# Kernel tuning notes

Measured on AMD Instinct MI355X. Metric: run time of the kernel, lower is better.

Reference implementation:

```python
import jax, jax.numpy as jnp
import numpy as np

B, Q_LEN, HID = 4, 1024, 4096
N_HEADS, N_KV_HEADS, HEAD_DIM = 32, 8, 128
PAST_LEN = 1024
SCALING = 1.0  # wrapper's self.scaling (applied to query before SDPA)
NEG = jnp.float32(-1e9)


def setup_inputs() -> dict:
    key = jax.random.key(0)
    ks = jax.random.split(key, 10)
    return {
        "hidden_states": jax.random.normal(ks[0], (B, Q_LEN, HID), jnp.float32),
        "past_k": jax.random.normal(ks[1], (B, N_KV_HEADS, PAST_LEN, HEAD_DIM), jnp.float32),
        "past_v": jax.random.normal(ks[2], (B, N_KV_HEADS, PAST_LEN, HEAD_DIM), jnp.float32),
        # attention_mask semantics follow the wrapper's SDPA path: positions where
        # attention_mask == 0 are attended (mask_bool True), others masked out.
        "attention_mask": jnp.zeros((B, PAST_LEN + Q_LEN), jnp.int32),
        "Wq": jax.random.normal(ks[3], (HID, HID), jnp.float32) * 0.02,
        "bq": jnp.zeros((HID,), jnp.float32),
        "Wk": jax.random.normal(ks[4], (N_KV_HEADS * HEAD_DIM, HID), jnp.float32) * 0.02,
        "bk": jnp.zeros((N_KV_HEADS * HEAD_DIM,), jnp.float32),
        "Wv": jax.random.normal(ks[5], (N_KV_HEADS * HEAD_DIM, HID), jnp.float32) * 0.02,
        "bv": jnp.zeros((N_KV_HEADS * HEAD_DIM,), jnp.float32),
        "Wo": jax.random.normal(ks[6], (HID, HID), jnp.float32) * 0.02,
        "bo": jnp.zeros((HID,), jnp.float32),
    }


def _shape(x, n_heads):
    # [B, S, n_heads*D] -> [B, n_heads, S, D]
    b, s, _ = x.shape
    return x.reshape(b, s, n_heads, HEAD_DIM).transpose(0, 2, 1, 3)


def reference(hidden_states, past_k, past_v, attention_mask,
              Wq, bq, Wk, bk, Wv, bv, Wo, bo):
    bsz, q_len, _ = hidden_states.shape
    # QKV projections (nn.Linear: x @ W.T + b)
    q = hidden_states @ Wq.T + bq
    k = hidden_states @ Wk.T + bk
    v = hidden_states @ Wv.T + bv
    q = q * SCALING
    q = _shape(q, N_HEADS)            # [B, H, Sq, D]
    k = _shape(k, N_KV_HEADS)         # [B, Hkv, Sq, D]
    v = _shape(v, N_KV_HEADS)
    # KV-cache concat along sequence dim
    k = jnp.concatenate([past_k, k], axis=2)   # [B, Hkv, Skv, D]
    v = jnp.concatenate([past_v, v], axis=2)
    kv_seq_len = k.shape[2]
    # GQA: repeat_interleave kv heads to match query heads
    groups = N_HEADS // N_KV_HEADS
    k = jnp.repeat(k, groups, axis=1)  # [B, H, Skv, D]
    v = jnp.repeat(v, groups, axis=1)
    # SDPA: scale 1/sqrt(head_dim), mask True = attend (wrapper's mask==0 path)
    scores = jnp.einsum("bhqd,bhkd->bhqk", q, k) / jnp.sqrt(jnp.float32(HEAD_DIM))
    attend = (attention_mask == 0)[:, None, None, :kv_seq_len]  # [B,1,1,Skv]
    scores = jnp.where(attend, scores, NEG)
    probs = jax.nn.softmax(scores, axis=-1)
    attn_out = jnp.einsum("bhqk,bhkd->bhqd", probs, v)  # [B, H, Sq, D]
    attn_out = attn_out.transpose(0, 2, 1, 3).reshape(bsz, q_len, N_HEADS * HEAD_DIM)
    return attn_out @ Wo.T + bo
```

## Files before the change

### kernel.cpp

```cpp
#include <hip/hip_runtime.h>
#include <cstdint>
#include <cstddef>

typedef __bf16 bf16;
typedef __bf16 bf16x8 __attribute__((ext_vector_type(8)));
typedef float  f32x4  __attribute__((ext_vector_type(4)));
typedef float  f32x16 __attribute__((ext_vector_type(16)));
typedef unsigned short u16x4v __attribute__((ext_vector_type(4)));
typedef unsigned int   u32x4v __attribute__((ext_vector_type(4)));

#define MFMA16(a, b, c) __builtin_amdgcn_mfma_f32_16x16x32_bf16((a), (b), (c), 0, 0, 0)
#define MFMA32(a, b, c) __builtin_amdgcn_mfma_f32_32x32x16_bf16((a), (b), (c), 0, 0, 0)

__device__ __forceinline__ void glds16(const bf16* g, bf16* l) {
    __builtin_amdgcn_global_load_lds(
        (__attribute__((address_space(1))) void*)(g),
        (__attribute__((address_space(3))) void*)(l), 16, 0, 0);
}

__device__ __forceinline__ unsigned cvtpk_bf16(float lo, float hi) {
    unsigned r;
    asm("v_cvt_pk_bf16_f32 %0, %1, %2" : "=v"(r) : "v"(lo), "v"(hi));
    return r;
}

__global__ __launch_bounds__(256) void cvt_bf16_k(const float* __restrict__ in,
                                                  bf16* __restrict__ out, long long n) {
    long long i = ((long long)blockIdx.x * 256 + threadIdx.x) * 8;
    if (i >= n) return;
    const float4* p = (const float4*)(in + i);
    float4 a = p[0], b = p[1];
    bf16x8 o;
    o[0] = (bf16)a.x; o[1] = (bf16)a.y; o[2] = (bf16)a.z; o[3] = (bf16)a.w;
    o[4] = (bf16)b.x; o[5] = (bf16)b.y; o[6] = (bf16)b.z; o[7] = (bf16)b.w;
    *(bf16x8*)(out + i) = o;
}

__global__ __launch_bounds__(256) void fused_cvt_k(const float* __restrict__ hidden,
                                                   const float* __restrict__ Wq,
                                                   const float* __restrict__ Wk,
                                                   const float* __restrict__ Wv,
                                                   const float* __restrict__ past_k,
                                                   bf16* __restrict__ Xb,
                                                   bf16* __restrict__ Wqb,
                                                   bf16* __restrict__ Wkvb,
                                                   bf16* __restrict__ Kb) {
    long long e = ((long long)blockIdx.x * 256 + threadIdx.x) * 8;
    const float* src;
    bf16* dst;
    if (e < 16777216ll) {
        src = hidden + e;           dst = Xb + e;
    } else if (e < 33554432ll) {
        long long i = e - 16777216ll;
        src = Wq + i;               dst = Wqb + i;
    } else if (e < 37748736ll) {
        long long i = e - 33554432ll;
        src = Wk + i;               dst = Wkvb + i;
    } else if (e < 41943040ll) {
        long long i = e - 37748736ll;
        src = Wv + i;               dst = Wkvb + 4194304ll + i;
    } else {
        long long i = e - 41943040ll;
        src = past_k + i;
        dst = Kb + (i >> 17) * 262144ll + (i & 131071ll);
    }
    const float4* p = (const float4*)src;
    float4 a = p[0], b = p[1];
    bf16x8 o;
    o[0] = (bf16)a.x; o[1] = (bf16)a.y; o[2] = (bf16)a.z; o[3] = (bf16)a.w;
    o[4] = (bf16)b.x; o[5] = (bf16)b.y; o[6] = (bf16)b.z; o[7] = (bf16)b.w;
    *(bf16x8*)dst = o;
}

__global__ __launch_bounds__(256) void cvt_pastv_k(const float* __restrict__ in,
                                                   bf16* __restrict__ Vt) {
    const int tid = blockIdx.x * 256 + threadIdx.x;
    const int d   = tid & 127;
    const int kv4 = (tid >> 7) & 255;
    const int bh  = tid >> 15;
    u16x4v pk;
#pragma unroll
    for (int r = 0; r < 4; ++r) {
        float v = in[((long long)bh * 1024 + kv4 * 4 + r) * 128 + d];
        pk[r] = __builtin_bit_cast(unsigned short, (bf16)v);
    }
    *(u16x4v*)(Vt + ((long long)bh * 128 + d) * 2048 + kv4 * 4) = pk;
}

__global__ __launch_bounds__(256) void gemm_kv(const bf16* __restrict__ A,
                                               const bf16* __restrict__ B,
                                               const float* __restrict__ bk,
                                               const float* __restrict__ bv,
                                               bf16* __restrict__ Kc,
                                               bf16* __restrict__ Vt,
                                               int K) {
    __shared__ bf16 Asm[128 * 32];
    __shared__ bf16 Bsm[128 * 32];
    const int t = threadIdx.x;
    const int lane = t & 63, w = t >> 6;
    const int quad = lane >> 4, l16 = lane & 15;
    const int wr = (w >> 1) * 64, wc = (w & 1) * 64;
    const long long m0 = (long long)blockIdx.y * 128, n0 = (long long)blockIdx.x * 128;

    f32x4 acc[4][4] = {};

    const int i1 = t, i2 = t + 256;
    const bf16* gA1 = A + (m0 + (i1 >> 2)) * K + (i1 & 3) * 8;
    const bf16* gA2 = A + (m0 + (i2 >> 2)) * K + (i2 & 3) * 8;
    const bf16* gB1 = B + (n0 + (i1 >> 2)) * K + (i1 & 3) * 8;
    const bf16* gB2 = B + (n0 + (i2 >> 2)) * K + (i2 & 3) * 8;
    bf16* lA1 = Asm + i1 * 8;
    bf16* lA2 = Asm + i2 * 8;
    bf16* lB1 = Bsm + i1 * 8;
    bf16* lB2 = Bsm + i2 * 8;

    for (int k0 = 0; k0 < K; k0 += 32) {
        glds16(gA1 + k0, lA1);
        glds16(gA2 + k0, lA2);
        glds16(gB1 + k0, lB1);
        glds16(gB2 + k0, lB2);
        __syncthreads();
        bf16x8 af[4], bfr[4];
#pragma unroll
        for (int i = 0; i < 4; ++i)
            af[i] = *(const bf16x8*)(Asm + (wr + i * 16 + l16) * 32 + quad * 8);
#pragma unroll
        for (int j = 0; j < 4; ++j)
            bfr[j] = *(const bf16x8*)(Bsm + (wc + j * 16 + l16) * 32 + quad * 8);
#pragma unroll
        for (int i = 0; i < 4; ++i)
#pragma unroll
            for (int j = 0; j < 4; ++j)
                acc[i][j] = MFMA16(af[i], bfr[j], acc[i][j]);
        __syncthreads();
    }

    const bool isK = (n0 < 1024);
    const long long c0 = isK ? n0 : (n0 - 1024);
    const float* bias = isK ? (bk + c0) : (bv + c0);

    float bs[4];
#pragma unroll
    for (int j = 0; j < 4; ++j) bs[j] = bias[wc + j * 16 + l16];

#pragma unroll
    for (int i = 0; i < 4; ++i) {
        const long long mbase = m0 + wr + i * 16 + quad * 4;
#pragma unroll
        for (int j = 0; j < 4; ++j) {
            const long long col = c0 + wc + j * 16 + l16;
            const int h = (int)(col >> 7), d = (int)(col & 127);
            if (isK) {
#pragma unroll
                for (int r = 0; r < 4; ++r) {
                    const long long m = mbase + r;
                    const long long bb = m >> 10, s = m & 1023;
                    Kc[((bb * 8 + h) * 2048 + 1024 + s) * 128 + d] = (bf16)(acc[i][j][r] + bs[j]);
                }
            } else {
                const long long bb = mbase >> 10, s = mbase & 1023;
                u16x4v pk;
#pragma unroll
                for (int r = 0; r < 4; ++r)
                    pk[r] = __builtin_bit_cast(unsigned short, (bf16)(acc[i][j][r] + bs[j]));
                *(u16x4v*)(Vt + ((bb * 8 + h) * 128 + d) * 2048 + 1024 + s) = pk;
            }
        }
    }
}

template <int MODE>
__global__ __launch_bounds__(512, 2) void gemm256(const bf16* __restrict__ A,
                                                  const bf16* __restrict__ B,
                                                  const float* __restrict__ bias,
                                                  void* __restrict__ Cv,
                                                  int M, int N, int K, float scale) {
    __shared__ bf16 S[4][16384];
    const int t = threadIdx.x, lane = t & 63, w = t >> 6;
    const int quad = lane >> 4, l16 = lane & 15;
    const int wm = w >> 2, wn = w & 3;

    const int nwg = gridDim.x * gridDim.y;
    const int bid = blockIdx.y * gridDim.x + blockIdx.x;
    const int lid = (bid & 7) * (nwg >> 3) + (bid >> 3);
    const long long m0 = (long long)(lid / gridDim.x) * 256;
    const long long n0 = (long long)(lid % gridDim.x) * 256;

    const int sA   = (lane & 7) ^ (lane >> 3);
    const int rsub = 2 * (lane >> 3) + (sA >> 2);
    const int colk = (sA & 3) * 8;
    const int c0 = w * 2, c1 = w * 2 + 1;
    const long long gA0 = (m0 + c0 * 16 + rsub) * (long long)K + colk;
    const long long gA1 = (m0 + c1 * 16 + rsub) * (long long)K + colk;
    const long long gB0 = (n0 + c0 * 16 + rsub) * (long long)K + colk;
    const long long gB1 = (n0 + c1 * 16 + rsub) * (long long)K + colk;

    const int lA7   = l16 >> 1;
    const int slotE = ((((l16 & 1) * 4 + quad) ^ lA7) * 16) >> 1;
    const int baseAe = (wm * 64 + lA7) * 64 + slotE;
    const int baseBe = (wn * 32 + lA7) * 64 + slotE;

    f32x4 acc[8][4] = {};

    auto stg = [&](int bufi, int tile) {
        const long long kk = (long long)tile * 32;
        bf16* sb = &S[bufi][0];
        glds16(A + gA0 + kk, sb + c0 * 512);
        glds16(A + gA1 + kk, sb + c1 * 512);
        glds16(B + gB0 + kk, sb + 8192 + c0 * 512);
        glds16(B + gB1 + kk, sb + 8192 + c1 * 512);
    };
    auto compute = [&](int tt) {
        const bf16* pA = &S[tt & 3][baseAe];
        const bf16* pB = &S[tt & 3][8192 + baseBe];
        bf16x8 af[8], bfr[4];
#pragma unroll
        for (int m = 0; m < 8; ++m) af[m] = *(const bf16x8*)(pA + m * 512);
#pragma unroll
        for (int n = 0; n < 4; ++n) bfr[n] = *(const bf16x8*)(pB + n * 512);
        __builtin_amdgcn_s_setprio(1);
#pragma unroll
        for (int m = 0; m < 8; ++m)
#pragma unroll
            for (int n = 0; n < 4; ++n)
                acc[m][n] = MFMA16(af[m], bfr[n], acc[m][n]);
        __builtin_amdgcn_s_setprio(0);
    };

    const int nt = K >> 5;

    stg(0, 0); stg(1, 1); stg(2, 2);
    asm volatile("s_waitcnt vmcnt(8)" ::: "memory");
    asm volatile("s_barrier" ::: "memory");

    for (int tt = 0; tt + 3 < nt; ++tt) {
        stg((tt + 3) & 3, tt + 3);
        compute(tt);
        asm volatile("s_waitcnt vmcnt(8)" ::: "memory");
        asm volatile("s_barrier" ::: "memory");
    }
    compute(nt - 3);
    asm volatile("s_waitcnt vmcnt(4)" ::: "memory");
    asm volatile("s_barrier" ::: "memory");
    compute(nt - 2);
    asm volatile("s_waitcnt vmcnt(0)" ::: "memory");
    asm volatile("s_barrier" ::: "memory");
    compute(nt - 1);

    float bs[4];
#pragma unroll
    for (int n = 0; n < 4; ++n) bs[n] = bias[n0 + wn * 64 + n * 16 + l16];

#pragma unroll
    for (int m = 0; m < 8; ++m) {
        const long long mbase = m0 + wm * 128 + m * 16 + quad * 4;
#pragma unroll
        for (int n = 0; n < 4; ++n) {
            const long long nn = n0 + wn * 64 + n * 16 + l16;
            if (MODE == 1) {
                float* Cf = (float*)Cv;
#pragma unroll
                for (int r = 0; r < 4; ++r)
                    Cf[(mbase + r) * N + nn] = acc[m][n][r] + bs[n];
            } else {
                bf16* Cq = (bf16*)Cv;
                const int h = (int)(nn >> 7), d = (int)(nn & 127);
#pragma unroll
                for (int r = 0; r < 4; ++r) {
                    const long long mr = mbase + r;
                    const long long bb = mr >> 10, s = mr & 1023;
                    Cq[((bb * 32 + h) * 1024 + s) * 128 + d] = (bf16)((acc[m][n][r] + bs[n]) * scale);
                }
            }
        }
    }
}

__global__ __launch_bounds__(512, 2) void attn_k(const bf16* __restrict__ Qs,
                                                 const bf16* __restrict__ Kc,
                                                 const bf16* __restrict__ Vt,
                                                 const int* __restrict__ amask,
                                                 bf16* __restrict__ AO) {
    const int phys = blockIdx.x;
    const int lid = (phys & 7) * 64 + (phys >> 3);
    const int qt = lid & 3, h = (lid >> 2) & 31, b = lid >> 7;
    const int hk = h >> 2;
    const int t = threadIdx.x, lane = t & 63, w = t >> 6;
    const int q32 = lane & 31, half = lane >> 5;

    __shared__ bf16 Ksm[2][64 * 128];
    __shared__ bf16 Vsm[2][128 * 64];
    __shared__ unsigned long long Msm[32];

    const bf16* kg = Kc + (long long)(b * 8 + hk) * 2048 * 128;
    const bf16* vg = Vt + (long long)(b * 8 + hk) * 128 * 2048;

    {
        const int* am = amask + b * 2048;
#pragma unroll
        for (int j = 0; j < 4; ++j) {
            unsigned long long bm = __ballot(am[w * 256 + j * 64 + lane] != 0);
            if (lane == 0) Msm[w * 4 + j] = bm;
        }
    }

    bf16x8 qf[8];
    {
        const bf16* qb = Qs + ((long long)(b * 32 + h) * 1024 + qt * 256 + w * 32 + q32) * 128 + half * 8;
#pragma unroll
        for (int kw = 0; kw < 8; ++kw) qf[kw] = *(const bf16x8*)(qb + kw * 16);
    }

    f32x16 Ot[4] = {};
    float mi = -1e30f, li = 0.f;

    const int krow = lane >> 4, kslot = lane & 15;
    const int vrow = lane >> 3, vslot = lane & 7;

#define STAGE(BUF, KV0) do {                                                                  \
        const int kr0 = w * 8 + krow;                                                         \
        glds16(kg + (long long)((KV0) + kr0) * 128 + ((kslot ^ (kr0 & 7)) * 8),               \
               &Ksm[BUF][(w * 8) * 128]);                                                     \
        const int kr1 = kr0 + 4;                                                              \
        glds16(kg + (long long)((KV0) + kr1) * 128 + ((kslot ^ (kr1 & 7)) * 8),               \
               &Ksm[BUF][(w * 8 + 4) * 128]);                                                 \
        const int vd0 = w * 16 + vrow;                                                        \
        glds16(vg + (long long)vd0 * 2048 + (KV0) + ((vslot ^ (vrow & 7)) * 8),               \
               &Vsm[BUF][(w * 16) * 64]);                                                     \
        const int vd1 = vd0 + 8;                                                              \
        glds16(vg + (long long)vd1 * 2048 + (KV0) + ((vslot ^ (vrow & 7)) * 8),               \
               &Vsm[BUF][(w * 16 + 8) * 64]);                                                 \
    } while (0)

    STAGE(0, 0);
    __syncthreads();

    int buf = 0;
    for (int tt = 0; tt < 32; ++tt) {
        if (tt < 31) STAGE(buf ^ 1, tt * 64 + 64);

        f32x16 s0 = {}, s1 = {};
        __builtin_amdgcn_s_setprio(1);
#pragma unroll
        for (int kw = 0; kw < 8; ++kw) {
            const int sl = ((kw * 2 + half) ^ (q32 & 7)) * 8;
            bf16x8 k0 = *(const bf16x8*)(&Ksm[buf][q32 * 128 + sl]);
            bf16x8 k1 = *(const bf16x8*)(&Ksm[buf][(32 + q32) * 128 + sl]);
            s0 = MFMA32(k0, qf[kw], s0);
            s1 = MFMA32(k1, qf[kw], s1);
        }
        __builtin_amdgcn_s_setprio(0);

        const unsigned long long mw = Msm[tt];
        if (mw) {
#pragma unroll
            for (int g = 0; g < 4; ++g)
#pragma unroll
                for (int j = 0; j < 4; ++j) {
                    const int kl = j + 8 * g + 4 * half;
                    if ((mw >> kl) & 1) s0[g * 4 + j] = -1e30f;
                    if ((mw >> (32 + kl)) & 1) s1[g * 4 + j] = -1e30f;
                }
        }

        float m0 = fmaxf(s0[0], s1[0]), m1 = fmaxf(s0[1], s1[1]);
        float m2 = fmaxf(s0[2], s1[2]), m3 = fmaxf(s0[3], s1[3]);
#pragma unroll
        for (int i = 4; i < 16; i += 4) {
            m0 = fmaxf(m0, fmaxf(s0[i + 0], s1[i + 0]));
            m1 = fmaxf(m1, fmaxf(s0[i + 1], s1[i + 1]));
            m2 = fmaxf(m2, fmaxf(s0[i + 2], s1[i + 2]));
            m3 = fmaxf(m3, fmaxf(s0[i + 3], s1[i + 3]));
        }
        float mx = fmaxf(fmaxf(m0, m1), fmaxf(m2, m3));
        {
            auto r = __builtin_amdgcn_permlane32_swap(__builtin_bit_cast(unsigned, mx),
                                                      __builtin_bit_cast(unsigned, mx), false, false);
            mx = fmaxf(mx, fmaxf(__builtin_bit_cast(float, (unsigned)r[0]),
                                 __builtin_bit_cast(float, (unsigned)r[1])));
        }

        if (__any(mx > mi + 8.f)) {
            const float mnew = fmaxf(mi, mx);
            const float al = exp2f(mi - mnew);
            mi = mnew;
            li *= al;
#pragma unroll
            for (int dt = 0; dt < 4; ++dt)
#pragma unroll
                for (int i = 0; i < 16; ++i) Ot[dt][i] *= al;
        }

        float a0 = 0.f, a1 = 0.f, a2 = 0.f, a3 = 0.f;
#pragma unroll
        for (int i = 0; i < 16; i += 4) {
            float p;
            p = exp2f(s0[i + 0] - mi); s0[i + 0] = p; a0 += p;
            p = exp2f(s0[i + 1] - mi); s0[i + 1] = p; a1 += p;
            p = exp2f(s0[i + 2] - mi); s0[i + 2] = p; a2 += p;
            p = exp2f(s0[i + 3] - mi); s0[i + 3] = p; a3 += p;
            p = exp2f(s1[i + 0] - mi); s1[i + 0] = p; a0 += p;
            p = exp2f(s1[i + 1] - mi); s1[i + 1] = p; a1 += p;
            p = exp2f(s1[i + 2] - mi); s1[i + 2] = p; a2 += p;
            p = exp2f(s1[i + 3] - mi); s1[i + 3] = p; a3 += p;
        }
        float sum = (a0 + a1) + (a2 + a3);
        {
            auto r = __builtin_amdgcn_permlane32_swap(__builtin_bit_cast(unsigned, sum),
                                                      __builtin_bit_cast(unsigned, sum), false, false);
            sum += __builtin_bit_cast(float, (unsigned)(half ? r[0] : r[1]));
        }
        li += sum;

        bf16x8 pf[4];
#pragma unroll
        for (int s32 = 0; s32 < 2; ++s32)
#pragma unroll
            for (int wp = 0; wp < 2; ++wp) {
                const f32x16& st = s32 ? s1 : s0;
                unsigned xa = cvtpk_bf16(st[8 * wp + 0], st[8 * wp + 1]);
                unsigned xb = cvtpk_bf16(st[8 * wp + 2], st[8 * wp + 3]);
                unsigned ya = cvtpk_bf16(st[8 * wp + 4], st[8 * wp + 5]);
                unsigned yb = cvtpk_bf16(st[8 * wp + 6], st[8 * wp + 7]);
                auto rA = __builtin_amdgcn_permlane32_swap(xa, ya, false, false);
                auto rB = __builtin_amdgcn_permlane32_swap(xb, yb, false, false);
                u32x4v fw;
                fw[0] = (unsigned)rA[0]; fw[1] = (unsigned)rB[0];
                fw[2] = (unsigned)rA[1]; fw[3] = (unsigned)rB[1];
                pf[s32 * 2 + wp] = __builtin_bit_cast(bf16x8, fw);
            }

        __builtin_amdgcn_s_setprio(1);
#pragma unroll
        for (int kvw = 0; kvw < 4; ++kvw) {
            const int sl = ((kvw * 2 + half) ^ (q32 & 7)) * 8;
#pragma unroll
            for (int dt = 0; dt < 4; ++dt) {
                bf16x8 vf = *(const bf16x8*)(&Vsm[buf][(dt * 32 + q32) * 64 + sl]);
                Ot[dt] = MFMA32(vf, pf[kvw], Ot[dt]);
            }
        }
        __builtin_amdgcn_s_setprio(0);

        __syncthreads();
        buf ^= 1;
    }
#undef STAGE

    const float inv = 1.f / li;
    const long long token = (long long)b * 1024 + qt * 256 + w * 32 + q32;
    bf16* ao = AO + token * 4096 + h * 128 + half * 4;
#pragma unroll
    for (int dt = 0; dt < 4; ++dt)
#pragma unroll
        for (int g = 0; g < 4; ++g) {
            u16x4v pk;
#pragma unroll
            for (int j = 0; j < 4; ++j)
                pk[j] = __builtin_bit_cast(unsigned short, (bf16)(Ot[dt][g * 4 + j] * inv));
            *(u16x4v*)(ao + dt * 32 + g * 8) = pk;
        }
}

extern "C" void kernel_launch(void* const* d_in, const int* in_sizes, int n_in,
                              void* d_out, int out_size, void* d_ws, size_t ws_size,
                              hipStream_t stream) {
    const float* hidden = (const float*)d_in[0];
    const float* past_k = (const float*)d_in[1];
    const float* past_v = (const float*)d_in[2];
    const int*   amask  = (const int*)d_in[3];
    const float* Wq = (const float*)d_in[4];
    const float* bq = (const float*)d_in[5];
    const float* Wk = (const float*)d_in[6];
    const float* bk = (const float*)d_in[7];
    const float* Wv = (const float*)d_in[8];
    const float* bv = (const float*)d_in[9];
    const float* Wo = (const float*)d_in[10];
    const float* bo = (const float*)d_in[11];

    char* ws = (char*)d_ws;
    bf16* Xb   = (bf16*)(ws);
    bf16* Wqb  = (bf16*)(ws + (1ll << 25));
    bf16* Wkvb = (bf16*)(ws + (1ll << 26));
    bf16* AOb  = (bf16*)(ws + (1ll << 26) + (1ll << 24));
    char* oc = (char*)d_out;
    bf16* Qb  = (bf16*)(oc);
    bf16* Kb  = (bf16*)(oc + (1ll << 25));
    bf16* Vtb = (bf16*)(oc + (1ll << 25) + (1ll << 24));

    const float qscale = 0.08838834764831845f * 1.44269504088896340f;

    fused_cvt_k<<<22528, 256, 0, stream>>>(hidden, Wq, Wk, Wv, past_k, Xb, Wqb, Wkvb, Kb);
    cvt_pastv_k<<<4096, 256, 0, stream>>>(past_v, Vtb);

    gemm256<4><<<dim3(16, 16), 512, 0, stream>>>(Xb, Wqb, bq, (void*)Qb, 4096, 4096, 4096, qscale);
    gemm_kv<<<dim3(16, 32), 256, 0, stream>>>(Xb, Wkvb, bk, bv, Kb, Vtb, 4096);

    cvt_bf16_k<<<8192, 256, 0, stream>>>(Wo, Wqb, 16777216ll);

    attn_k<<<512, 512, 0, stream>>>(Qb, Kb, Vtb, amask, AOb);

    gemm256<1><<<dim3(16, 16), 512, 0, stream>>>(AOb, Wqb, bo, d_out, 4096, 4096, 4096, 1.0f);
}
```

Measured before the change: 796.1 us.

## Split attention softmax into halves with lazy max rescale, smaller blocks, LDS-transposed V conversion

The attention kernel moves from 512-thread blocks covering 256 queries to 256-thread blocks covering 128 queries, so twice as many blocks run with four waves each. The per-tile online softmax no longer computes a row max before exponentiating. It exponentiates against a running offset, interleaves the exp/convert of each 32-key half with its PV MFMAs, and rescales only when a probability exceeds a threshold. This removes a reduction and barrier-like dependency from the critical path, but risks overflow or precision loss if scores jump sharply. The past_v transpose kernel now stages through shared memory to get coalesced reads and writes.

```diff
diff --git a/kernel.cpp b/kernel.cpp
--- a/kernel.cpp
+++ b/kernel.cpp
@@ -74,17 +74,31 @@
 
 __global__ __launch_bounds__(256) void cvt_pastv_k(const float* __restrict__ in,
                                                    bf16* __restrict__ Vt) {
-    const int tid = blockIdx.x * 256 + threadIdx.x;
-    const int d   = tid & 127;
-    const int kv4 = (tid >> 7) & 255;
-    const int bh  = tid >> 15;
-    u16x4v pk;
-#pragma unroll
-    for (int r = 0; r < 4; ++r) {
-        float v = in[((long long)bh * 1024 + kv4 * 4 + r) * 128 + d];
-        pk[r] = __builtin_bit_cast(unsigned short, (bf16)v);
-    }
-    *(u16x4v*)(Vt + ((long long)bh * 128 + d) * 2048 + kv4 * 4) = pk;
+    __shared__ bf16 T[128][72];
+    const int t = threadIdx.x;
+    const int bh = blockIdx.x >> 4, kb = blockIdx.x & 15;
+    const int r  = t >> 2;
+    const int c0 = (t & 3) * 32;
+    const float* src = in + ((long long)bh * 1024 + kb * 64 + r) * 128 + c0;
+#pragma unroll
+    for (int i = 0; i < 8; ++i) {
+        float4 f = *(const float4*)(src + i * 4);
+        T[c0 + i * 4 + 0][r] = (bf16)f.x;
+        T[c0 + i * 4 + 1][r] = (bf16)f.y;
+        T[c0 + i * 4 + 2][r] = (bf16)f.z;
+        T[c0 + i * 4 + 3][r] = (bf16)f.w;
+    }
+    __syncthreads();
+    const int d = t >> 1, ho = (t & 1) * 32;
+    bf16* dst = Vt + ((long long)bh * 128 + d) * 2048 + kb * 64 + ho;
+#pragma unroll
+    for (int j = 0; j < 8; ++j) {
+        u16x4v pk;
+#pragma unroll
+        for (int q = 0; q < 4; ++q)
+            pk[q] = __builtin_bit_cast(unsigned short, T[d][ho + j * 4 + q]);
+        *(u16x4v*)(dst + j * 4) = pk;
+    }
 }
 
 __global__ __launch_bounds__(256) void gemm_kv(const bf16* __restrict__ A,
@@ -276,14 +290,14 @@
     }
 }
 
-__global__ __launch_bounds__(512, 2) void attn_k(const bf16* __restrict__ Qs,
+__global__ __launch_bounds__(256, 2) void attn_k(const bf16* __restrict__ Qs,
                                                  const bf16* __restrict__ Kc,
                                                  const bf16* __restrict__ Vt,
                                                  const int* __restrict__ amask,
                                                  bf16* __restrict__ AO) {
     const int phys = blockIdx.x;
-    const int lid = (phys & 7) * 64 + (phys >> 3);
-    const int qt = lid & 3, h = (lid >> 2) & 31, b = lid >> 7;
+    const int lid = (phys & 7) * 128 + (phys >> 3);
+    const int qt = lid & 7, h = (lid >> 3) & 31, b = lid >> 8;
     const int hk = h >> 2;
     const int t = threadIdx.x, lane = t & 63, w = t >> 6;
     const int q32 = lane & 31, half = lane >> 5;
@@ -298,38 +312,38 @@
     {
         const int* am = amask + b * 2048;
 #pragma unroll
-        for (int j = 0; j < 4; ++j) {
-            unsigned long long bm = __ballot(am[w * 256 + j * 64 + lane] != 0);
-            if (lane == 0) Msm[w * 4 + j] = bm;
+        for (int j = 0; j < 8; ++j) {
+            unsigned long long bm = __ballot(am[(w * 8 + j) * 64 + lane] != 0);
+            if (lane == 0) Msm[w * 8 + j] = bm;
         }
     }
 
     bf16x8 qf[8];
     {
-        const bf16* qb = Qs + ((long long)(b * 32 + h) * 1024 + qt * 256 + w * 32 + q32) * 128 + half * 8;
+        const bf16* qb = Qs + ((long long)(b * 32 + h) * 1024 + qt * 128 + w * 32 + q32) * 128 + half * 8;
 #pragma unroll
         for (int kw = 0; kw < 8; ++kw) qf[kw] = *(const bf16x8*)(qb + kw * 16);
     }
 
     f32x16 Ot[4] = {};
-    float mi = -1e30f, li = 0.f;
+    float mi = 0.f, li = 0.f;
 
     const int krow = lane >> 4, kslot = lane & 15;
     const int vrow = lane >> 3, vslot = lane & 7;
 
 #define STAGE(BUF, KV0) do {                                                                  \
-        const int kr0 = w * 8 + krow;                                                         \
-        glds16(kg + (long long)((KV0) + kr0) * 128 + ((kslot ^ (kr0 & 7)) * 8),               \
-               &Ksm[BUF][(w * 8) * 128]);                                                     \
-        const int kr1 = kr0 + 4;                                                              \
-        glds16(kg + (long long)((KV0) + kr1) * 128 + ((kslot ^ (kr1 & 7)) * 8),               \
-               &Ksm[BUF][(w * 8 + 4) * 128]);                                                 \
-        const int vd0 = w * 16 + vrow;                                                        \
-        glds16(vg + (long long)vd0 * 2048 + (KV0) + ((vslot ^ (vrow & 7)) * 8),               \
-               &Vsm[BUF][(w * 16) * 64]);                                                     \
-        const int vd1 = vd0 + 8;                                                              \
-        glds16(vg + (long long)vd1 * 2048 + (KV0) + ((vslot ^ (vrow & 7)) * 8),               \
-               &Vsm[BUF][(w * 16 + 8) * 64]);                                                 \
+        _Pragma("unroll")                                                                     \
+        for (int i = 0; i < 4; ++i) {                                                         \
+            const int kr = w * 16 + i * 4 + krow;                                             \
+            glds16(kg + (long long)((KV0) + kr) * 128 + ((kslot ^ (kr & 7)) * 8),             \
+                   &Ksm[BUF][(w * 16 + i * 4) * 128]);                                        \
+        }                                                                                     \
+        _Pragma("unroll")                                                                     \
+        for (int i = 0; i < 4; ++i) {                                                         \
+            const int vd = w * 32 + i * 8 + vrow;                                             \
+            glds16(vg + (long long)vd * 2048 + (KV0) + ((vslot ^ (vrow & 7)) * 8),            \
+                   &Vsm[BUF][(w * 32 + i * 8) * 64]);                                         \
+        }                                                                                     \
     } while (0)
 
     STAGE(0, 0);
@@ -337,7 +351,8 @@
 
     int buf = 0;
     for (int tt = 0; tt < 32; ++tt) {
-        if (tt < 31) STAGE(buf ^ 1, tt * 64 + 64);
+        if (tt < 31) STAGE(buf ^ 1, (tt + 1) * 64);
+        const unsigned long long mw = Msm[tt];
 
         f32x16 s0 = {}, s1 = {};
         __builtin_amdgcn_s_setprio(1);
@@ -345,65 +360,104 @@
         for (int kw = 0; kw < 8; ++kw) {
             const int sl = ((kw * 2 + half) ^ (q32 & 7)) * 8;
             bf16x8 k0 = *(const bf16x8*)(&Ksm[buf][q32 * 128 + sl]);
+            s0 = MFMA32(k0, qf[kw], s0);
+        }
+#pragma unroll
+        for (int kw = 0; kw < 8; ++kw) {
+            const int sl = ((kw * 2 + half) ^ (q32 & 7)) * 8;
             bf16x8 k1 = *(const bf16x8*)(&Ksm[buf][(32 + q32) * 128 + sl]);
-            s0 = MFMA32(k0, qf[kw], s0);
             s1 = MFMA32(k1, qf[kw], s1);
         }
         __builtin_amdgcn_s_setprio(0);
 
-        const unsigned long long mw = Msm[tt];
+        float a0 = 0.f, a1 = 0.f, a2 = 0.f, a3 = 0.f;
+        float p0 = 0.f, p1 = 0.f, p2 = 0.f, p3 = 0.f;
+        bf16x8 pf[4];
+
+#pragma unroll
+        for (int i = 0; i < 16; ++i) s0[i] = exp2f(s0[i] - mi);
         if (mw) {
 #pragma unroll
             for (int g = 0; g < 4; ++g)
 #pragma unroll
-                for (int j = 0; j < 4; ++j) {
-                    const int kl = j + 8 * g + 4 * half;
-                    if ((mw >> kl) & 1) s0[g * 4 + j] = -1e30f;
-                    if ((mw >> (32 + kl)) & 1) s1[g * 4 + j] = -1e30f;
-                }
-        }
-
-        float m0 = fmaxf(s0[0], s1[0]), m1 = fmaxf(s0[1], s1[1]);
-        float m2 = fmaxf(s0[2], s1[2]), m3 = fmaxf(s0[3], s1[3]);
-#pragma unroll
-        for (int i = 4; i < 16; i += 4) {
-            m0 = fmaxf(m0, fmaxf(s0[i + 0], s1[i + 0]));
-            m1 = fmaxf(m1, fmaxf(s0[i + 1], s1[i + 1]));
-            m2 = fmaxf(m2, fmaxf(s0[i + 2], s1[i + 2]));
-            m3 = fmaxf(m3, fmaxf(s0[i + 3], s1[i + 3]));
-        }
-        float mx = fmaxf(fmaxf(m0, m1), fmaxf(m2, m3));
-        {
-            auto r = __builtin_amdgcn_permlane32_swap(__builtin_bit_cast(unsigned, mx),
-                                                      __builtin_bit_cast(unsigned, mx), false, false);
-            mx = fmaxf(mx, fmaxf(__builtin_bit_cast(float, (unsigned)r[0]),
-                                 __builtin_bit_cast(float, (unsigned)r[1])));
-        }
-
-        if (__any(mx > mi + 8.f)) {
-            const float mnew = fmaxf(mi, mx);
-            const float al = exp2f(mi - mnew);
-            mi = mnew;
-            li *= al;
-#pragma unroll
-            for (int dt = 0; dt < 4; ++dt)
-#pragma unroll
-                for (int i = 0; i < 16; ++i) Ot[dt][i] *= al;
-        }
-
-        float a0 = 0.f, a1 = 0.f, a2 = 0.f, a3 = 0.f;
+                for (int j = 0; j < 4; ++j)
+                    if ((mw >> (j + 8 * g + 4 * half)) & 1) s0[g * 4 + j] = 0.f;
+        }
 #pragma unroll
         for (int i = 0; i < 16; i += 4) {
-            float p;
-            p = exp2f(s0[i + 0] - mi); s0[i + 0] = p; a0 += p;
-            p = exp2f(s0[i + 1] - mi); s0[i + 1] = p; a1 += p;
-            p = exp2f(s0[i + 2] - mi); s0[i + 2] = p; a2 += p;
-            p = exp2f(s0[i + 3] - mi); s0[i + 3] = p; a3 += p;
-            p = exp2f(s1[i + 0] - mi); s1[i + 0] = p; a0 += p;
-            p = exp2f(s1[i + 1] - mi); s1[i + 1] = p; a1 += p;
-            p = exp2f(s1[i + 2] - mi); s1[i + 2] = p; a2 += p;
-            p = exp2f(s1[i + 3] - mi); s1[i + 3] = p; a3 += p;
-        }
+            a0 += s0[i + 0]; p0 = fmaxf(p0, s0[i + 0]);
+            a1 += s0[i + 1]; p1 = fmaxf(p1, s0[i + 1]);
+            a2 += s0[i + 2]; p2 = fmaxf(p2, s0[i + 2]);
+            a3 += s0[i + 3]; p3 = fmaxf(p3, s0[i + 3]);
+        }
+#pragma unroll
+        for (int wp = 0; wp < 2; ++wp) {
+            unsigned xa = cvtpk_bf16(s0[8 * wp + 0], s0[8 * wp + 1]);
+            unsigned xb = cvtpk_bf16(s0[8 * wp + 2], s0[8 * wp + 3]);
+            unsigned ya = cvtpk_bf16(s0[8 * wp + 4], s0[8 * wp + 5]);
+            unsigned yb = cvtpk_bf16(s0[8 * wp + 6], s0[8 * wp + 7]);
+            auto rA = __builtin_amdgcn_permlane32_swap(xa, ya, false, false);
+            auto rB = __builtin_amdgcn_permlane32_swap(xb, yb, false, false);
+            u32x4v fw;
+            fw[0] = (unsigned)rA[0]; fw[1] = (unsigned)rB[0];
+            fw[2] = (unsigned)rA[1]; fw[3] = (unsigned)rB[1];
+            pf[wp] = __builtin_bit_cast(bf16x8, fw);
+        }
+
+        __builtin_amdgcn_s_setprio(1);
+#pragma unroll
+        for (int kvw = 0; kvw < 2; ++kvw) {
+            const int sl = ((kvw * 2 + half) ^ (q32 & 7)) * 8;
+#pragma unroll
+            for (int dt = 0; dt < 4; ++dt) {
+                bf16x8 vf = *(const bf16x8*)(&Vsm[buf][(dt * 32 + q32) * 64 + sl]);
+                Ot[dt] = MFMA32(vf, pf[kvw], Ot[dt]);
+            }
+        }
+        __builtin_amdgcn_s_setprio(0);
+
+#pragma unroll
+        for (int i = 0; i < 16; ++i) s1[i] = exp2f(s1[i] - mi);
+        if (mw) {
+#pragma unroll
+            for (int g = 0; g < 4; ++g)
+#pragma unroll
+                for (int j = 0; j < 4; ++j)
+                    if ((mw >> (32 + j + 8 * g + 4 * half)) & 1) s1[g * 4 + j] = 0.f;
+        }
+#pragma unroll
+        for (int i = 0; i < 16; i += 4) {
+            a0 += s1[i + 0]; p0 = fmaxf(p0, s1[i + 0]);
+            a1 += s1[i + 1]; p1 = fmaxf(p1, s1[i + 1]);
+            a2 += s1[i + 2]; p2 = fmaxf(p2, s1[i + 2]);
+            a3 += s1[i + 3]; p3 = fmaxf(p3, s1[i + 3]);
+        }
+#pragma unroll
+        for (int wp = 0; wp < 2; ++wp) {
+            unsigned xa = cvtpk_bf16(s1[8 * wp + 0], s1[8 * wp + 1]);
+            unsigned xb = cvtpk_bf16(s1[8 * wp + 2], s1[8 * wp + 3]);
+            unsigned ya = cvtpk_bf16(s1[8 * wp + 4], s1[8 * wp + 5]);
+            unsigned yb = cvtpk_bf16(s1[8 * wp + 6], s1[8 * wp + 7]);
+            auto rA = __builtin_amdgcn_permlane32_swap(xa, ya, false, false);
+            auto rB = __builtin_amdgcn_permlane32_swap(xb, yb, false, false);
+            u32x4v fw;
+            fw[0] = (unsigned)rA[0]; fw[1] = (unsigned)rB[0];
+            fw[2] = (unsigned)rA[1]; fw[3] = (unsigned)rB[1];
+            pf[2 + wp] = __builtin_bit_cast(bf16x8, fw);
+        }
+
+        __builtin_amdgcn_s_setprio(1);
+#pragma unroll
+        for (int kvw = 2; kvw < 4; ++kvw) {
+            const int sl = ((kvw * 2 + half) ^ (q32 & 7)) * 8;
+#pragma unroll
+            for (int dt = 0; dt < 4; ++dt) {
+                bf16x8 vf = *(const bf16x8*)(&Vsm[buf][(dt * 32 + q32) * 64 + sl]);
+                Ot[dt] = MFMA32(vf, pf[kvw], Ot[dt]);
+            }
+        }
+        __builtin_amdgcn_s_setprio(0);
+
         float sum = (a0 + a1) + (a2 + a3);
         {
             auto r = __builtin_amdgcn_permlane32_swap(__builtin_bit_cast(unsigned, sum),
@@ -411,36 +465,23 @@
             sum += __builtin_bit_cast(float, (unsigned)(half ? r[0] : r[1]));
         }
         li += sum;
-
-        bf16x8 pf[4];
-#pragma unroll
-        for (int s32 = 0; s32 < 2; ++s32)
-#pragma unroll
-            for (int wp = 0; wp < 2; ++wp) {
-                const f32x16& st = s32 ? s1 : s0;
-                unsigned xa = cvtpk_bf16(st[8 * wp + 0], st[8 * wp + 1]);
-                unsigned xb = cvtpk_bf16(st[8 * wp + 2], st[8 * wp + 3]);
-                unsigned ya = cvtpk_bf16(st[8 * wp + 4], st[8 * wp + 5]);
-                unsigned yb = cvtpk_bf16(st[8 * wp + 6], st[8 * wp + 7]);
-                auto rA = __builtin_amdgcn_permlane32_swap(xa, ya, false, false);
-                auto rB = __builtin_amdgcn_permlane32_swap(xb, yb, false, false);
-                u32x4v fw;
-                fw[0] = (unsigned)rA[0]; fw[1] = (unsigned)rB[0];
-                fw[2] = (unsigned)rA[1]; fw[3] = (unsigned)rB[1];
-                pf[s32 * 2 + wp] = __builtin_bit_cast(bf16x8, fw);
-            }
-
-        __builtin_amdgcn_s_setprio(1);
-#pragma unroll
-        for (int kvw = 0; kvw < 4; ++kvw) {
-            const int sl = ((kvw * 2 + half) ^ (q32 & 7)) * 8;
-#pragma unroll
-            for (int dt = 0; dt < 4; ++dt) {
-                bf16x8 vf = *(const bf16x8*)(&Vsm[buf][(dt * 32 + q32) * 64 + sl]);
-                Ot[dt] = MFMA32(vf, pf[kvw], Ot[dt]);
-            }
-        }
-        __builtin_amdgcn_s_setprio(0);
+        float pm = fmaxf(fmaxf(p0, p1), fmaxf(p2, p3));
+        {
+            auto r = __builtin_amdgcn_permlane32_swap(__builtin_bit_cast(unsigned, pm),
+                                                      __builtin_bit_cast(unsigned, pm), false, false);
+            pm = fmaxf(pm, fmaxf(__builtin_bit_cast(float, (unsigned)r[0]),
+                                 __builtin_bit_cast(float, (unsigned)r[1])));
+        }
+        if (__any(pm > 256.f)) {
+            const float al  = pm > 1.f ? 1.f / pm : 1.f;
+            const float dmi = pm > 1.f ? log2f(pm) : 0.f;
+            mi += dmi;
+            li *= al;
+#pragma unroll
+            for (int dt = 0; dt < 4; ++dt)
+#pragma unroll
+                for (int i = 0; i < 16; ++i) Ot[dt][i] *= al;
+        }
 
         __syncthreads();
         buf ^= 1;
@@ -448,7 +489,7 @@
 #undef STAGE
 
     const float inv = 1.f / li;
-    const long long token = (long long)b * 1024 + qt * 256 + w * 32 + q32;
+    const long long token = (long long)b * 1024 + qt * 128 + w * 32 + q32;
     bf16* ao = AO + token * 4096 + h * 128 + half * 4;
 #pragma unroll
     for (int dt = 0; dt < 4; ++dt)
@@ -491,14 +532,14 @@
     const float qscale = 0.08838834764831845f * 1.44269504088896340f;
 
     fused_cvt_k<<<22528, 256, 0, stream>>>(hidden, Wq, Wk, Wv, past_k, Xb, Wqb, Wkvb, Kb);
-    cvt_pastv_k<<<4096, 256, 0, stream>>>(past_v, Vtb);
+    cvt_pastv_k<<<512, 256, 0, stream>>>(past_v, Vtb);
 
     gemm256<4><<<dim3(16, 16), 512, 0, stream>>>(Xb, Wqb, bq, (void*)Qb, 4096, 4096, 4096, qscale);
     gemm_kv<<<dim3(16, 32), 256, 0, stream>>>(Xb, Wkvb, bk, bv, Kb, Vtb, 4096);
 
     cvt_bf16_k<<<8192, 256, 0, stream>>>(Wo, Wqb, 16777216ll);
 
-    attn_k<<<512, 512, 0, stream>>>(Qb, Kb, Vtb, amask, AOb);
+    attn_k<<<1024, 256, 0, stream>>>(Qb, Kb, Vtb, amask, AOb);
 
     gemm256<1><<<dim3(16, 16), 512, 0, stream>>>(AOb, Wqb, bo, d_out, 4096, 4096, 4096, 1.0f);
 }
```

Result: no change. 798.3 us (+0.3%).
